# Kernel optimization log

Hardware: AMD Instinct MI355X
Metric: run time of the kernel (lower is better)

Reference implementation:

```python
import jax, jax.numpy as jnp
import numpy as np

VOCAB, EMB = 5000, 300
UNITS = [256, 512, 256]  # two return_sequences layers + final return-last layer
DENSE = 64


def lstm_layer(x, W, U, b, return_seq):
    """Keras-style LSTM with activation='relu', recurrent_activation='sigmoid'.
    x: [B,T,D]; W: [D,4u]; U: [u,4u]; b: [4u]. Gate order: i, f, c, o."""
    B = x.shape[0]
    u = U.shape[0]
    xg = jnp.einsum('btd,dg->btg', x, W) + b  # precompute input projections [B,T,4u]

    def step(carry, xg_t):
        h, c = carry
        g = xg_t + h @ U
        i, f, cc, o = jnp.split(g, 4, axis=-1)
        i = jax.nn.sigmoid(i)
        f = jax.nn.sigmoid(f)
        o = jax.nn.sigmoid(o)
        c = f * c + i * jax.nn.relu(cc)
        h = o * jax.nn.relu(c)
        return (h, c), h

    h0 = jnp.zeros((B, u), x.dtype)
    (hT, _), hs = jax.lax.scan(step, (h0, h0), jnp.swapaxes(xg, 0, 1))
    return jnp.swapaxes(hs, 0, 1) if return_seq else hT


def setup_inputs() -> dict:
    key = jax.random.key(0)
    ks = iter(jax.random.split(key, 16))
    s = 0.05  # small init keeps relu-LSTM numerically stable
    inp = {
        'tokens': jax.random.randint(next(ks), (128, 512), 0, VOCAB, dtype=jnp.int32),
        'emb': jax.random.normal(next(ks), (VOCAB, EMB), jnp.float32) * s,
    }
    d = EMB
    for li, u in enumerate(UNITS):
        inp[f'W{li}'] = jax.random.normal(next(ks), (d, 4 * u), jnp.float32) * s
        inp[f'U{li}'] = jax.random.normal(next(ks), (u, 4 * u), jnp.float32) * s
        inp[f'b{li}'] = jnp.zeros((4 * u,), jnp.float32)
        d = u
    inp['Wd'] = jax.random.normal(next(ks), (UNITS[-1], DENSE), jnp.float32) * s
    inp['bd'] = jnp.zeros((DENSE,), jnp.float32)
    inp['Wc'] = jax.random.normal(next(ks), (DENSE, 1), jnp.float32) * s
    inp['bc'] = jnp.zeros((1,), jnp.float32)
    return inp


def reference(tokens, emb, W0, U0, b0, W1, U1, b1, W2, U2, b2, Wd, bd, Wc, bc):
    x = emb[tokens]                                   # [B,T,300]
    x = lstm_layer(x, W0, U0, b0, return_seq=True)    # [B,T,256]
    x = lstm_layer(x, W1, U1, b1, return_seq=True)    # [B,T,512]
    x = lstm_layer(x, W2, U2, b2, return_seq=False)   # [B,256]
    x = jax.nn.relu(x @ Wd + bd)                      # [B,64]
    return jax.nn.sigmoid(x @ Wc + bc)                # [B,1]
```

## Files before the change

### kernel.cpp

```cpp
#include <hip/hip_runtime.h>
#include <cstdint>
#include <cstddef>

#define BATCH  128
#define SEQT   512
#define EMB_D  300
#define VOCABN 5000
#define KP0    320
#define NU0    256
#define NU1    512
#define NU2    256
#define NDENSE 64
#define RING   32
#define LIM    (1 << 19)

typedef unsigned short ushortT;
typedef unsigned long long ull;
typedef __attribute__((ext_vector_type(8))) short bf16x8;
typedef __attribute__((ext_vector_type(8))) unsigned short u16x8;
typedef __attribute__((ext_vector_type(4))) unsigned short u16x4;
typedef __attribute__((ext_vector_type(4))) float f32x4;

#define AGT __HIP_MEMORY_SCOPE_AGENT

static __device__ __forceinline__ unsigned short f2bf(float x) {
    union { float f; unsigned u; } v; v.f = x;
    const unsigned r = v.u + 0x7FFFu + ((v.u >> 16) & 1u);
    return (unsigned short)(r >> 16);
}
static __device__ __forceinline__ float bf2f(unsigned short b) {
    union { unsigned u; float f; } v; v.u = ((unsigned)b) << 16;
    return v.f;
}
static __device__ __forceinline__ float sigmoidf_(float x) {
    return 1.f / (1.f + __expf(-x));
}
static __device__ __forceinline__ unsigned ald(const unsigned* p) {
    return __hip_atomic_load((unsigned*)p, __ATOMIC_RELAXED, AGT);
}
static __device__ __forceinline__ void ast(unsigned* p, unsigned v) {
    __hip_atomic_store(p, v, __ATOMIC_RELAXED, AGT);
}
static __device__ __forceinline__ void ld16c(u16x8* d, const void* p) {
    asm volatile("global_load_dwordx4 %0, %1, off sc0 sc1"
                 : "=&v"(*d) : "v"(p) : "memory");
}
static __device__ __forceinline__ void ld8c(u16x4* d, const void* p) {
    asm volatile("global_load_dwordx2 %0, %1, off sc0 sc1"
                 : "=&v"(*d) : "v"(p) : "memory");
}
static __device__ __forceinline__ void st4c(void* p, unsigned v) {
    asm volatile("global_store_dword %0, %1, off sc0 sc1"
                 :: "v"(p), "v"(v) : "memory");
}
static __device__ __forceinline__ void wait0() {
    asm volatile("s_waitcnt vmcnt(0)" ::: "memory");
    __builtin_amdgcn_sched_barrier(0);
}
static __device__ __forceinline__ void wait1() {
    asm volatile("s_waitcnt vmcnt(1)" ::: "memory");
    __builtin_amdgcn_sched_barrier(0);
}

__global__ __launch_bounds__(256) void convert_WT(
    const float* __restrict__ W, ushortT* __restrict__ WbfT,
    int K, int NG, int KP, int total)
{
    for (int idx = blockIdx.x * 256 + threadIdx.x; idx < total; idx += gridDim.x * 256) {
        const int m = idx / KP, k = idx - m * KP;
        WbfT[idx] = (k < K) ? f2bf(W[(size_t)k * NG + m]) : (ushortT)0;
    }
}
__global__ __launch_bounds__(256) void convert_emb(
    const float* __restrict__ emb, ushortT* __restrict__ embbf)
{
    const int total = VOCABN * KP0;
    for (int idx = blockIdx.x * 256 + threadIdx.x; idx < total; idx += gridDim.x * 256) {
        const int v = idx / KP0, k = idx - v * KP0;
        embbf[idx] = (k < EMB_D) ? f2bf(emb[(size_t)v * EMB_D + k]) : (ushortT)0;
    }
}

__global__ __launch_bounds__(256) void gemm_xg0(
    const ushortT* __restrict__ embbf,
    const int*   __restrict__ tokens,
    const ushortT* __restrict__ W0T,
    const float* __restrict__ bias,
    ushortT* __restrict__ xg0)
{
    __shared__ ushortT Wl[128][32];
    __shared__ ushortT Xl[128][32];
    __shared__ int tokL[128];

    const int tid = threadIdx.x;
    const int t   = blockIdx.x;
    const int m0  = blockIdx.y * 128;
    const int wv  = tid >> 6;
    const int lane = tid & 63;
    const int lo  = lane & 15;
    const int hi  = lane >> 4;

    if (tid < 128) tokL[tid] = tokens[tid * SEQT + t];
    __syncthreads();

    f32x4 acc[2][8];
    #pragma unroll
    for (int s = 0; s < 2; ++s)
        #pragma unroll
        for (int n = 0; n < 8; ++n)
            acc[s][n] = f32x4{0.f, 0.f, 0.f, 0.f};

    for (int k0 = 0; k0 < KP0; k0 += 32) {
        #pragma unroll
        for (int it = 0; it < 2; ++it) {
            const int idx = tid + it * 256;
            const int row = idx >> 2, gq = idx & 3;
            const int gs  = gq ^ ((row >> 1) & 3);
            *(u16x8*)&Wl[row][gs * 8] =
                *(const u16x8*)(W0T + (size_t)(m0 + row) * KP0 + k0 + gq * 8);
            *(u16x8*)&Xl[row][gs * 8] =
                *(const u16x8*)(embbf + (size_t)tokL[row] * KP0 + k0 + gq * 8);
        }
        __syncthreads();

        bf16x8 bfr[8];
        #pragma unroll
        for (int n = 0; n < 8; ++n) {
            const int row = n * 16 + lo;
            bfr[n] = *(const bf16x8*)&Xl[row][(hi ^ ((row >> 1) & 3)) * 8];
        }
        #pragma unroll
        for (int s = 0; s < 2; ++s) {
            const int row = wv * 32 + s * 16 + lo;
            const bf16x8 a = *(const bf16x8*)&Wl[row][(hi ^ ((row >> 1) & 3)) * 8];
            #pragma unroll
            for (int n = 0; n < 8; ++n)
                acc[s][n] = __builtin_amdgcn_mfma_f32_16x16x32_bf16(a, bfr[n], acc[s][n], 0, 0, 0);
        }
        __syncthreads();
    }

    #pragma unroll
    for (int s = 0; s < 2; ++s)
        #pragma unroll
        for (int j = 0; j < 4; ++j) {
            const int m = m0 + wv * 32 + s * 16 + hi * 4 + j;
            const float bi = bias[m];
            #pragma unroll
            for (int n = 0; n < 8; ++n)
                xg0[(((size_t)t * 8 + n) * 1024 + m) * 16 + lo] = f2bf(acc[s][n][j] + bi);
        }
}

template<int U_, int JCOLS, bool XATOMIC>
__device__ void rec_role(
    int rid,
    const float* __restrict__ Umat,
    const ushortT* __restrict__ xgring, int xmask,
    ushortT* __restrict__ hring,
    unsigned* Fown,
    unsigned* Xown, int xph, int xmsh,
    unsigned* Xguard, int nGd,
    char* smem)
{
    constexpr int NGu   = 4 * U_;
    constexpr int WPG   = U_ / JCOLS;
    constexpr int JH    = JCOLS / 2;
    constexpr int TILES = JH / 16;
    constexpr int KT    = U_ / 32;
    constexpr int GR    = U_ / 8;
    constexpr int NLD   = (16 * GR) / 512;

    ushortT* hstage = (ushortT*)smem;
    float*   ex     = (float*)(smem + 2 * 16 * U_);

    const int tid = threadIdx.x, w = tid >> 6, lane = tid & 63;
    const int lo = lane & 15, hi = lane >> 4;
    const int g4 = w & 3, chh = w >> 2;
    const int grp = rid & 7, wgj = rid >> 3;
    const int b0 = grp * 16, J = wgj * JCOLS;
    const size_t S = (size_t)128 * U_;

    int gc[TILES];
    #pragma unroll
    for (int tl = 0; tl < TILES; ++tl)
        gc[tl] = g4 * U_ + J + chh * JH + tl * 16 + lo;

    bf16x8 bfr[TILES][KT];
    #pragma unroll
    for (int tl = 0; tl < TILES; ++tl)
        #pragma unroll
        for (int kt = 0; kt < KT; ++kt) {
            const float* up = Umat + (size_t)(kt * 32 + hi * 8) * NGu + gc[tl];
            bf16x8 v;
            #pragma unroll
            for (int i = 0; i < 8; ++i) v[i] = (short)f2bf(up[(size_t)i * NGu]);
            bfr[tl][kt] = v;
        }

    float creg[TILES][4];
    #pragma unroll
    for (int tl = 0; tl < TILES; ++tl)
        #pragma unroll
        for (int r = 0; r < 4; ++r) creg[tl][r] = 0.f;

    for (int t = 0; t < SEQT; ++t) {
        if (w == 0) {
            if (t > 0) {
                int guard = 0; bool ok;
                do {
                    bool pred = true;
                    if (lane < 2 * WPG)
                        pred = ((int)ald(&Fown[(grp * 2 * WPG + lane) * 16]) >= t);
                    ok = __all(pred);
                    if (!ok) __builtin_amdgcn_s_sleep(1);
                } while (!ok && ++guard < LIM);
            }
            {
                int guard = 0; bool ok;
                do {
                    bool pred = true;
                    if (XATOMIC && lane < 4) {
                        const int mt = (lane * U_ + J) >> xmsh;
                        const int fi = mt * xph + (t & (xph - 1));
                        pred = ((int)ald(&Xown[fi * 16]) >= t + 1);
                    }
                    for (int i = lane; i < nGd; i += 64)
                        pred = pred && ((int)ald(&Xguard[i * 16]) >= t - (RING - 1));
                    ok = __all(pred);
                    if (!ok) __builtin_amdgcn_s_sleep(8);
                } while (!ok && ++guard < LIM);
            }
        }
        __syncthreads();

        u16x4 xr[TILES];
        const size_t xb = (size_t)((t & xmask) * 8 + grp) * NGu;
        if (XATOMIC) {
            #pragma unroll
            for (int tl = 0; tl < TILES; ++tl)
                ld8c(&xr[tl], xgring + (xb + gc[tl]) * 16 + hi * 4);
        } else {
            #pragma unroll
            for (int tl = 0; tl < TILES; ++tl)
                xr[tl] = *(const u16x4*)(xgring + (xb + gc[tl]) * 16 + hi * 4);
        }
        u16x8 hr[NLD];
        int di[NLD];
        if (t > 0) {
            const ushortT* hsrc = hring + (size_t)((t - 1) & (RING - 1)) * S;
            #pragma unroll
            for (int q = 0; q < NLD; ++q) {
                const int i = tid + q * 512;
                const int row = i / GR, gi = i - row * GR;
                ld16c(&hr[q], hsrc + (size_t)(b0 + row) * U_ + gi * 8);
                di[q] = (row * GR + (gi ^ (row & 7))) * 8;
            }
        }
        if (XATOMIC || t > 0) wait0();
        if (t > 0) {
            #pragma unroll
            for (int q = 0; q < NLD; ++q)
                *(u16x8*)&hstage[di[q]] = hr[q];
        }
        __syncthreads();

        f32x4 acc[TILES];
        #pragma unroll
        for (int tl = 0; tl < TILES; ++tl) acc[tl] = f32x4{0.f, 0.f, 0.f, 0.f};
        if (t > 0) {
            #pragma unroll
            for (int kt = 0; kt < KT; ++kt) {
                const int gs = (kt * 4 + hi) ^ (lo & 7);
                const bf16x8 a = *(const bf16x8*)&hstage[(lo * GR + gs) * 8];
                #pragma unroll
                for (int tl = 0; tl < TILES; ++tl)
                    acc[tl] = __builtin_amdgcn_mfma_f32_16x16x32_bf16(a, bfr[tl][kt], acc[tl], 0, 0, 0);
            }
        }

        float p[TILES][4];
        #pragma unroll
        for (int tl = 0; tl < TILES; ++tl)
            #pragma unroll
            for (int r = 0; r < 4; ++r)
                p[tl][r] = acc[tl][r] + bf2f(xr[tl][r]);

        if (g4 != 2) {
            const int slot = (g4 == 3) ? 2 : g4;
            #pragma unroll
            for (int tl = 0; tl < TILES; ++tl)
                #pragma unroll
                for (int r = 0; r < 4; ++r)
                    ex[((slot * 2 + chh) * JH + tl * 16 + lo) * 17 + hi * 4 + r] = sigmoidf_(p[tl][r]);
        }
        __syncthreads();

        if (g4 == 2) {
            ushortT* hwr = hring + (size_t)(t & (RING - 1)) * S;
            #pragma unroll
            for (int tl = 0; tl < TILES; ++tl) {
                const int jh = tl * 16 + lo;
                const int j  = gc[tl] - 2 * U_;
                unsigned own[4], oth[4];
                #pragma unroll
                for (int r = 0; r < 4; ++r) {
                    const int row = hi * 4 + r;
                    const float i_ = ex[((0 * 2 + chh) * JH + jh) * 17 + row];
                    const float f_ = ex[((1 * 2 + chh) * JH + jh) * 17 + row];
                    const float o_ = ex[((2 * 2 + chh) * JH + jh) * 17 + row];
                    creg[tl][r] = f_ * creg[tl][r] + i_ * fmaxf(p[tl][r], 0.f);
                    const float hn = o_ * fmaxf(creg[tl][r], 0.f);
                    own[r] = (unsigned)f2bf(hn);
                }
                #pragma unroll
                for (int r = 0; r < 4; ++r)
                    oth[r] = (unsigned)__shfl_xor((int)own[r], 1);
                const int odd = lo & 1;
                const int rb = odd ? 2 : 0;
                const int je = j - odd;
                #pragma unroll
                for (int q = 0; q < 2; ++q) {
                    const int r = rb + q;
                    const unsigned pk = odd ? (oth[r] | (own[r] << 16))
                                            : (own[r] | (oth[r] << 16));
                    st4c(&hwr[(size_t)(b0 + hi * 4 + r) * U_ + je], pk);
                }
            }
            wait0();
            if (lane == 0)
                ast(&Fown[((grp * WPG + wgj) * 2 + chh) * 16], (unsigned)(t + 1));
        }
    }
}

template<int MC, int NGATES, int KP, int P>
__device__ void worker_role(
    int mtile, int phase,
    const ushortT* __restrict__ WT,
    const float* __restrict__ bias,
    const ushortT* __restrict__ hring,
    ushortT* __restrict__ xgring,
    unsigned* Fup, int nUp,
    unsigned* Fguard, int nGd,
    unsigned* Xrel,
    char* smem)
{
    constexpr int GR2 = KP / 8;
    constexpr int NIT = KP / 32;
    constexpr int WR  = MC / 8;
    constexpr int MT  = WR / 16;
    ushortT* Wl = (ushortT*)smem;
    ushortT* Xl = (ushortT*)(smem + (size_t)MC * KP * 2);

    const int tid = threadIdx.x, w = tid >> 6, lane = tid & 63;
    const int lo = lane & 15, hi = lane >> 4;
    const int m0 = mtile * MC;
    const int row = tid >> 2, gq = tid & 3;
    const int gsx = gq ^ ((row >> 1) & 3);

    for (int i = tid; i < MC * GR2; i += 512) {
        const int r_ = i / GR2, gi = i - r_ * GR2;
        const int gs = gi ^ (r_ & 7);
        *(u16x8*)&Wl[(r_ * GR2 + gs) * 8] =
            *(const u16x8*)(WT + (size_t)(m0 + r_) * KP + gi * 8);
    }
    float bv[MT][4];
    #pragma unroll
    for (int mt = 0; mt < MT; ++mt)
        #pragma unroll
        for (int j = 0; j < 4; ++j)
            bv[mt][j] = bias[m0 + w * WR + mt * 16 + hi * 4 + j];
    __syncthreads();

    for (int t = phase; t < SEQT; t += P) {
        if (w == 0) {
            int guard = 0; bool ok;
            do {
                bool pred = true;
                for (int i = lane; i < nUp; i += 64)
                    pred = pred && ((int)ald(&Fup[i * 16]) >= t + 1);
                for (int i = lane; i < nGd; i += 64)
                    pred = pred && ((int)ald(&Fguard[i * 16]) >= t - (RING - 1));
                ok = __all(pred);
                if (!ok) __builtin_amdgcn_s_sleep(32);
            } while (!ok && ++guard < LIM);
        }
        __syncthreads();

        const ushortT* hslab = hring + (size_t)(t & (RING - 1)) * 128 * KP;

        f32x4 acc[MT][8];
        #pragma unroll
        for (int mt = 0; mt < MT; ++mt)
            #pragma unroll
            for (int nn = 0; nn < 8; ++nn) acc[mt][nn] = f32x4{0.f, 0.f, 0.f, 0.f};

        u16x8 Ra, Rb;
        ld16c(&Ra, hslab + (size_t)row * KP + gq * 8);
        #pragma unroll
        for (int it = 0; it < NIT; ++it) {
            const bool even = ((it & 1) == 0);
            if (it + 1 < NIT) {
                ld16c(even ? &Rb : &Ra, hslab + (size_t)row * KP + (it + 1) * 32 + gq * 8);
                wait1();
            } else {
                wait0();
            }
            ushortT* Xc = Xl + (it & 1) * (128 * 32);
            *(u16x8*)&Xc[row * 32 + gsx * 8] = even ? Ra : Rb;
            __syncthreads();
            const int k0 = it * 32;
            #pragma unroll
            for (int mt = 0; mt < MT; ++mt) {
                const int arow = w * WR + mt * 16 + lo;
                const int gsa = ((k0 >> 3) + hi) ^ (arow & 7);
                const bf16x8 a = *(const bf16x8*)&Wl[(arow * GR2 + gsa) * 8];
                #pragma unroll
                for (int nn = 0; nn < 8; ++nn) {
                    const int brow = nn * 16 + lo;
                    const bf16x8 b = *(const bf16x8*)&Xc[brow * 32 + (hi ^ ((brow >> 1) & 3)) * 8];
                    acc[mt][nn] = __builtin_amdgcn_mfma_f32_16x16x32_bf16(a, b, acc[mt][nn], 0, 0, 0);
                }
            }
            __syncthreads();
        }

        const size_t slab = (size_t)(t & (RING - 1)) * 8;
        #pragma unroll
        for (int mt = 0; mt < MT; ++mt) {
            #pragma unroll
            for (int nn = 0; nn < 8; ++nn) {
                const int b = nn * 16 + lo;
                unsigned own[4], oth[4];
                #pragma unroll
                for (int j = 0; j < 4; ++j)
                    own[j] = (unsigned)f2bf(acc[mt][nn][j] + bv[mt][j]);
                #pragma unroll
                for (int j = 0; j < 4; ++j)
                    oth[j] = (unsigned)__shfl_xor((int)own[j], 1);
                const int odd = lo & 1;
                const int jb = odd ? 2 : 0;
                const int be = (b & 15) - odd;
                #pragma unroll
                for (int q = 0; q < 2; ++q) {
                    const int j = jb + q;
                    const int m = m0 + w * WR + mt * 16 + hi * 4 + j;
                    const unsigned pk = odd ? (oth[j] | (own[j] << 16))
                                            : (own[j] | (oth[j] << 16));
                    st4c(&xgring[((slab + nn) * NGATES + m) * 16 + be], pk);
                }
            }
        }
        wait0();
        __syncthreads();
        if (tid == 0)
            ast(Xrel, (unsigned)(t + 1));
    }
}

struct MegaArgs {
    const float *U0, *U1, *U2;
    const ushortT *W1T, *W2T;
    const float *b1, *b2;
    const ushortT* xg0;
    ushortT *xg1, *xg2;
    ushortT *h0r, *h1r, *h2r;
    unsigned *F0, *F1, *F2, *X1, *X2;
};

__global__ __launch_bounds__(512, 1) void mega(MegaArgs A)
{
    extern __shared__ char smem[];
    const int bid = blockIdx.x;
    if (bid < 16) {
        rec_role<NU0, 128, false>(bid, A.U0, A.xg0, 511, A.h0r, A.F0,
                                  nullptr, 1, 0, A.X1, 64, smem);
    } else if (bid < 80) {
        rec_role<NU1, 64, true>(bid - 16, A.U1, A.xg1, RING - 1, A.h1r, A.F1,
                                A.X1, 8, 8, A.X2, 32, smem);
    } else if (bid < 96) {
        rec_role<NU2, 128, true>(bid - 80, A.U2, A.xg2, RING - 1, A.h2r, A.F2,
                                 A.X2, 4, 7, nullptr, 0, smem);
    } else if (bid < 160) {
        const int wid = bid - 96;
        const int mt = wid & 7, ph = wid >> 3;
        worker_role<256, 2048, 256, 8>(mt, ph, A.W1T, A.b1, A.h0r, A.xg1,
                                       A.F0, 32, A.F1, 128, A.X1 + (mt * 8 + ph) * 16, smem);
    } else {
        const int wid = bid - 160;
        const int mt = wid & 7, ph = wid >> 3;
        worker_role<128, 1024, 512, 4>(mt, ph, A.W2T, A.b2, A.h1r, A.xg2,
                                       A.F1, 128, A.F2, 32, A.X2 + (mt * 4 + ph) * 16, smem);
    }
}

__global__ __launch_bounds__(64) void head_kernel(
    const ushortT* __restrict__ h2,
    const float* __restrict__ Wd,
    const float* __restrict__ bd,
    const float* __restrict__ Wc,
    const float* __restrict__ bc,
    float* __restrict__ out)
{
    const int b = blockIdx.x;
    const int j = threadIdx.x;
    float a = bd[j];
    const ushortT* hrow = h2 + (size_t)b * NU2;
    #pragma unroll 4
    for (int k = 0; k < NU2; ++k)
        a += bf2f(hrow[k]) * Wd[(size_t)k * NDENSE + j];
    a = fmaxf(a, 0.f) * Wc[j];
    #pragma unroll
    for (int off = 32; off > 0; off >>= 1)
        a += __shfl_down(a, off);
    if (j == 0)
        out[b] = 1.f / (1.f + expf(-(a + bc[0])));
}

extern "C" void kernel_launch(void* const* d_in, const int* in_sizes, int n_in,
                              void* d_out, int out_size, void* d_ws, size_t ws_size,
                              hipStream_t stream)
{
    const int*   tokens = (const int*)  d_in[0];
    const float* emb    = (const float*)d_in[1];
    const float* W0     = (const float*)d_in[2];
    const float* Ur0    = (const float*)d_in[3];
    const float* b0v    = (const float*)d_in[4];
    const float* W1     = (const float*)d_in[5];
    const float* Ur1    = (const float*)d_in[6];
    const float* b1v    = (const float*)d_in[7];
    const float* W2     = (const float*)d_in[8];
    const float* Ur2    = (const float*)d_in[9];
    const float* b2v    = (const float*)d_in[10];
    const float* Wd     = (const float*)d_in[11];
    const float* bd     = (const float*)d_in[12];
    const float* Wc     = (const float*)d_in[13];
    const float* bc     = (const float*)d_in[14];
    float* out = (float*)d_out;

    char* p = (char*)d_ws;
    auto alloc = [&](size_t bytes) -> char* {
        char* q = p; p += (bytes + 255) & ~(size_t)255; return q;
    };
    ushortT* xg0   = (ushortT*)alloc((size_t)SEQT * 8 * 1024 * 16 * 2);
    ushortT* xg1   = (ushortT*)alloc((size_t)RING * 8 * 2048 * 16 * 2);
    ushortT* xg2   = (ushortT*)alloc((size_t)RING * 8 * 1024 * 16 * 2);
    ushortT* h0r   = (ushortT*)alloc((size_t)RING * 128 * NU0 * 2);
    ushortT* h1r   = (ushortT*)alloc((size_t)RING * 128 * NU1 * 2);
    ushortT* h2r   = (ushortT*)alloc((size_t)RING * 128 * NU2 * 2);
    ushortT* W0T   = (ushortT*)alloc((size_t)1024 * KP0 * 2);
    ushortT* W1T   = (ushortT*)alloc((size_t)2048 * NU0 * 2);
    ushortT* W2T   = (ushortT*)alloc((size_t)1024 * NU1 * 2);
    ushortT* embbf = (ushortT*)alloc((size_t)VOCABN * KP0 * 2);
    unsigned* flg  = (unsigned*)alloc(32768);

    unsigned* F0 = flg;
    unsigned* F1 = F0 + 32 * 16;
    unsigned* F2 = F1 + 128 * 16;
    unsigned* X1 = F2 + 32 * 16;
    unsigned* X2 = X1 + 64 * 16;

    hipMemsetAsync(flg, 0, 32768, stream);

    convert_WT<<<512, 256, 0, stream>>>(W0, W0T, EMB_D, 1024, KP0, 1024 * KP0);
    convert_WT<<<512, 256, 0, stream>>>(W1, W1T, NU0, 2048, NU0, 2048 * NU0);
    convert_WT<<<512, 256, 0, stream>>>(W2, W2T, NU1, 1024, NU1, 1024 * NU1);
    convert_emb<<<1024, 256, 0, stream>>>(emb, embbf);

    gemm_xg0<<<dim3(SEQT, 8), 256, 0, stream>>>(embbf, tokens, W0T, b0v, xg0);

    MegaArgs A;
    A.U0 = Ur0; A.U1 = Ur1; A.U2 = Ur2;
    A.W1T = W1T; A.W2T = W2T;
    A.b1 = b1v; A.b2 = b2v;
    A.xg0 = xg0; A.xg1 = xg1; A.xg2 = xg2;
    A.h0r = h0r; A.h1r = h1r; A.h2r = h2r;
    A.F0 = F0; A.F1 = F1; A.F2 = F2; A.X1 = X1; A.X2 = X2;

    void* args[] = {&A};
    hipLaunchCooperativeKernel((void*)mega, dim3(192), dim3(512), args, 147456, stream);

    head_kernel<<<BATCH, 64, 0, stream>>>(h2r + (size_t)31 * 128 * NU2,
                                          Wd, bd, Wc, bc, out);
}
```

Baseline: 2.813 ms.

## Restructure recurrent blocks so each wave owns all four gates per column

Each recurrent workgroup shrinks to 256 threads and 64 hidden columns, and each wave now computes all four gate tiles for its 16 columns. The cell update happens in registers, with no LDS exchange of sigmoid values and no extra barrier. The input-projection slice for step t+1 is prefetched during step t and the X-flag poll is merged into the single per-step wait loop. The grid grows from 192 to 224 blocks, and the workers are adjusted to 256 threads with two loads per thread and flag counts halved. This trades more blocks and more cross-block flag polling for a shorter per-step critical path within each block.

```diff
diff --git a/kernel.cpp b/kernel.cpp
--- a/kernel.cpp
+++ b/kernel.cpp
@@ -57,8 +57,8 @@
     asm volatile("s_waitcnt vmcnt(0)" ::: "memory");
     __builtin_amdgcn_sched_barrier(0);
 }
-static __device__ __forceinline__ void wait1() {
-    asm volatile("s_waitcnt vmcnt(1)" ::: "memory");
+static __device__ __forceinline__ void wait2() {
+    asm volatile("s_waitcnt vmcnt(2)" ::: "memory");
     __builtin_amdgcn_sched_barrier(0);
 }
 
@@ -152,185 +152,169 @@
         }
 }
 
-template<int U_, int JCOLS, bool XATOMIC>
+template<int U_, bool XATOMIC, int XTSH, int XPH>
 __device__ void rec_role(
     int rid,
     const float* __restrict__ Umat,
     const ushortT* __restrict__ xgring, int xmask,
     ushortT* __restrict__ hring,
     unsigned* Fown,
-    unsigned* Xown, int xph, int xmsh,
+    unsigned* Xown,
     unsigned* Xguard, int nGd,
     char* smem)
 {
-    constexpr int NGu   = 4 * U_;
-    constexpr int WPG   = U_ / JCOLS;
-    constexpr int JH    = JCOLS / 2;
-    constexpr int TILES = JH / 16;
-    constexpr int KT    = U_ / 32;
-    constexpr int GR    = U_ / 8;
-    constexpr int NLD   = (16 * GR) / 512;
+    constexpr int NGu = 4 * U_;
+    constexpr int WPG = U_ / 64;
+    constexpr int KT  = U_ / 32;
+    constexpr int GR  = U_ / 8;
+    constexpr int NLD = (16 * GR) / 256;
 
     ushortT* hstage = (ushortT*)smem;
-    float*   ex     = (float*)(smem + 2 * 16 * U_);
 
     const int tid = threadIdx.x, w = tid >> 6, lane = tid & 63;
     const int lo = lane & 15, hi = lane >> 4;
-    const int g4 = w & 3, chh = w >> 2;
     const int grp = rid & 7, wgj = rid >> 3;
-    const int b0 = grp * 16, J = wgj * JCOLS;
+    const int b0 = grp * 16, J = wgj * 64;
+    const int jcol = J + w * 16 + lo;
     const size_t S = (size_t)128 * U_;
 
-    int gc[TILES];
+    bf16x8 bfr[4][KT];
     #pragma unroll
-    for (int tl = 0; tl < TILES; ++tl)
-        gc[tl] = g4 * U_ + J + chh * JH + tl * 16 + lo;
-
-    bf16x8 bfr[TILES][KT];
-    #pragma unroll
-    for (int tl = 0; tl < TILES; ++tl)
+    for (int g = 0; g < 4; ++g)
         #pragma unroll
         for (int kt = 0; kt < KT; ++kt) {
-            const float* up = Umat + (size_t)(kt * 32 + hi * 8) * NGu + gc[tl];
+            const float* up = Umat + (size_t)(kt * 32 + hi * 8) * NGu + g * U_ + jcol;
             bf16x8 v;
             #pragma unroll
             for (int i = 0; i < 8; ++i) v[i] = (short)f2bf(up[(size_t)i * NGu]);
-            bfr[tl][kt] = v;
-        }
-
-    float creg[TILES][4];
-    #pragma unroll
-    for (int tl = 0; tl < TILES; ++tl)
-        #pragma unroll
-        for (int r = 0; r < 4; ++r) creg[tl][r] = 0.f;
+            bfr[g][kt] = v;
+        }
+
+    float creg[4] = {0.f, 0.f, 0.f, 0.f};
+
+    if (XATOMIC) {
+        if (w == 0) {
+            int guard = 0; bool ok;
+            do {
+                bool pred = true;
+                if (lane < 4) {
+                    const int mt = (lane * U_ + J) >> XTSH;
+                    pred = ((int)ald(&Xown[(mt * XPH) * 16]) >= 1);
+                }
+                ok = __all(pred);
+                if (!ok) __builtin_amdgcn_s_sleep(2);
+            } while (!ok && ++guard < LIM);
+        }
+        __syncthreads();
+    }
+    u16x4 xnext[4];
+    {
+        const size_t xb = (size_t)grp * NGu;
+        #pragma unroll
+        for (int g = 0; g < 4; ++g) {
+            const ushortT* ap = xgring + (xb + g * U_ + jcol) * 16 + hi * 4;
+            if (XATOMIC) ld8c(&xnext[g], ap);
+            else         xnext[g] = *(const u16x4*)ap;
+        }
+        if (XATOMIC) wait0();
+    }
 
     for (int t = 0; t < SEQT; ++t) {
         if (w == 0) {
-            if (t > 0) {
-                int guard = 0; bool ok;
-                do {
-                    bool pred = true;
-                    if (lane < 2 * WPG)
-                        pred = ((int)ald(&Fown[(grp * 2 * WPG + lane) * 16]) >= t);
-                    ok = __all(pred);
-                    if (!ok) __builtin_amdgcn_s_sleep(1);
-                } while (!ok && ++guard < LIM);
-            }
-            {
-                int guard = 0; bool ok;
-                do {
-                    bool pred = true;
-                    if (XATOMIC && lane < 4) {
-                        const int mt = (lane * U_ + J) >> xmsh;
-                        const int fi = mt * xph + (t & (xph - 1));
-                        pred = ((int)ald(&Xown[fi * 16]) >= t + 1);
-                    }
-                    for (int i = lane; i < nGd; i += 64)
-                        pred = pred && ((int)ald(&Xguard[i * 16]) >= t - (RING - 1));
-                    ok = __all(pred);
-                    if (!ok) __builtin_amdgcn_s_sleep(8);
-                } while (!ok && ++guard < LIM);
-            }
-        }
-        __syncthreads();
-
-        u16x4 xr[TILES];
-        const size_t xb = (size_t)((t & xmask) * 8 + grp) * NGu;
-        if (XATOMIC) {
-            #pragma unroll
-            for (int tl = 0; tl < TILES; ++tl)
-                ld8c(&xr[tl], xgring + (xb + gc[tl]) * 16 + hi * 4);
-        } else {
-            #pragma unroll
-            for (int tl = 0; tl < TILES; ++tl)
-                xr[tl] = *(const u16x4*)(xgring + (xb + gc[tl]) * 16 + hi * 4);
-        }
+            int guard = 0; bool ok;
+            do {
+                bool pred = true;
+                if (t > 0 && lane < WPG)
+                    pred = ((int)ald(&Fown[(grp * WPG + lane) * 16]) >= t);
+                if (XATOMIC && t + 1 < SEQT && lane < 4) {
+                    const int mt = (lane * U_ + J) >> XTSH;
+                    const int fi = mt * XPH + ((t + 1) & (XPH - 1));
+                    pred = pred && ((int)ald(&Xown[fi * 16]) >= t + 2);
+                }
+                for (int i = lane; i < nGd; i += 64)
+                    pred = pred && ((int)ald(&Xguard[i * 16]) >= t - (RING - 1));
+                ok = __all(pred);
+                if (!ok) __builtin_amdgcn_s_sleep(1);
+            } while (!ok && ++guard < LIM);
+        }
+        __syncthreads();
+
+        u16x4 xcur[4];
+        #pragma unroll
+        for (int g = 0; g < 4; ++g) xcur[g] = xnext[g];
+
         u16x8 hr[NLD];
-        int di[NLD];
         if (t > 0) {
             const ushortT* hsrc = hring + (size_t)((t - 1) & (RING - 1)) * S;
             #pragma unroll
             for (int q = 0; q < NLD; ++q) {
-                const int i = tid + q * 512;
+                const int i = tid + q * 256;
                 const int row = i / GR, gi = i - row * GR;
                 ld16c(&hr[q], hsrc + (size_t)(b0 + row) * U_ + gi * 8);
-                di[q] = (row * GR + (gi ^ (row & 7))) * 8;
-            }
-        }
-        if (XATOMIC || t > 0) wait0();
-        if (t > 0) {
-            #pragma unroll
-            for (int q = 0; q < NLD; ++q)
-                *(u16x8*)&hstage[di[q]] = hr[q];
-        }
-        __syncthreads();
-
-        f32x4 acc[TILES];
-        #pragma unroll
-        for (int tl = 0; tl < TILES; ++tl) acc[tl] = f32x4{0.f, 0.f, 0.f, 0.f};
+            }
+            wait0();
+            #pragma unroll
+            for (int q = 0; q < NLD; ++q) {
+                const int i = tid + q * 256;
+                const int row = i / GR, gi = i - row * GR;
+                *(u16x8*)&hstage[(row * GR + (gi ^ (row & 7))) * 8] = hr[q];
+            }
+        }
+        if (t + 1 < SEQT) {
+            const size_t xb = (size_t)(((t + 1) & xmask) * 8 + grp) * NGu;
+            #pragma unroll
+            for (int g = 0; g < 4; ++g) {
+                const ushortT* ap = xgring + (xb + g * U_ + jcol) * 16 + hi * 4;
+                if (XATOMIC) ld8c(&xnext[g], ap);
+                else         xnext[g] = *(const u16x4*)ap;
+            }
+        }
+        __syncthreads();
+
+        f32x4 acc[4];
+        #pragma unroll
+        for (int g = 0; g < 4; ++g) acc[g] = f32x4{0.f, 0.f, 0.f, 0.f};
         if (t > 0) {
             #pragma unroll
             for (int kt = 0; kt < KT; ++kt) {
                 const int gs = (kt * 4 + hi) ^ (lo & 7);
                 const bf16x8 a = *(const bf16x8*)&hstage[(lo * GR + gs) * 8];
                 #pragma unroll
-                for (int tl = 0; tl < TILES; ++tl)
-                    acc[tl] = __builtin_amdgcn_mfma_f32_16x16x32_bf16(a, bfr[tl][kt], acc[tl], 0, 0, 0);
-            }
-        }
-
-        float p[TILES][4];
-        #pragma unroll
-        for (int tl = 0; tl < TILES; ++tl)
-            #pragma unroll
-            for (int r = 0; r < 4; ++r)
-                p[tl][r] = acc[tl][r] + bf2f(xr[tl][r]);
-
-        if (g4 != 2) {
-            const int slot = (g4 == 3) ? 2 : g4;
-            #pragma unroll
-            for (int tl = 0; tl < TILES; ++tl)
-                #pragma unroll
-                for (int r = 0; r < 4; ++r)
-                    ex[((slot * 2 + chh) * JH + tl * 16 + lo) * 17 + hi * 4 + r] = sigmoidf_(p[tl][r]);
-        }
-        __syncthreads();
-
-        if (g4 == 2) {
-            ushortT* hwr = hring + (size_t)(t & (RING - 1)) * S;
-            #pragma unroll
-            for (int tl = 0; tl < TILES; ++tl) {
-                const int jh = tl * 16 + lo;
-                const int j  = gc[tl] - 2 * U_;
-                unsigned own[4], oth[4];
-                #pragma unroll
-                for (int r = 0; r < 4; ++r) {
-                    const int row = hi * 4 + r;
-                    const float i_ = ex[((0 * 2 + chh) * JH + jh) * 17 + row];
-                    const float f_ = ex[((1 * 2 + chh) * JH + jh) * 17 + row];
-                    const float o_ = ex[((2 * 2 + chh) * JH + jh) * 17 + row];
-                    creg[tl][r] = f_ * creg[tl][r] + i_ * fmaxf(p[tl][r], 0.f);
-                    const float hn = o_ * fmaxf(creg[tl][r], 0.f);
-                    own[r] = (unsigned)f2bf(hn);
-                }
-                #pragma unroll
-                for (int r = 0; r < 4; ++r)
-                    oth[r] = (unsigned)__shfl_xor((int)own[r], 1);
-                const int odd = lo & 1;
-                const int rb = odd ? 2 : 0;
-                const int je = j - odd;
-                #pragma unroll
-                for (int q = 0; q < 2; ++q) {
-                    const int r = rb + q;
-                    const unsigned pk = odd ? (oth[r] | (own[r] << 16))
-                                            : (own[r] | (oth[r] << 16));
-                    st4c(&hwr[(size_t)(b0 + hi * 4 + r) * U_ + je], pk);
-                }
-            }
-            wait0();
-            if (lane == 0)
-                ast(&Fown[((grp * WPG + wgj) * 2 + chh) * 16], (unsigned)(t + 1));
-        }
+                for (int g = 0; g < 4; ++g)
+                    acc[g] = __builtin_amdgcn_mfma_f32_16x16x32_bf16(a, bfr[g][kt], acc[g], 0, 0, 0);
+            }
+        }
+
+        ushortT* hwr = hring + (size_t)(t & (RING - 1)) * S;
+        unsigned own[4], oth[4];
+        #pragma unroll
+        for (int r = 0; r < 4; ++r) {
+            const float i_ = sigmoidf_(acc[0][r] + bf2f(xcur[0][r]));
+            const float f_ = sigmoidf_(acc[1][r] + bf2f(xcur[1][r]));
+            const float cc = fmaxf(acc[2][r] + bf2f(xcur[2][r]), 0.f);
+            const float o_ = sigmoidf_(acc[3][r] + bf2f(xcur[3][r]));
+            creg[r] = f_ * creg[r] + i_ * cc;
+            own[r] = (unsigned)f2bf(o_ * fmaxf(creg[r], 0.f));
+        }
+        #pragma unroll
+        for (int r = 0; r < 4; ++r)
+            oth[r] = (unsigned)__shfl_xor((int)own[r], 1);
+        {
+            const int odd = lo & 1;
+            const int rb = odd ? 2 : 0;
+            const int je = jcol - odd;
+            #pragma unroll
+            for (int q = 0; q < 2; ++q) {
+                const int r = rb + q;
+                const unsigned pk = odd ? (oth[r] | (own[r] << 16))
+                                        : (own[r] | (oth[r] << 16));
+                st4c(&hwr[(size_t)(b0 + hi * 4 + r) * U_ + je], pk);
+            }
+        }
+        wait0();
+        __syncthreads();
+        if (tid == 0)
+            ast(&Fown[(grp * WPG + wgj) * 16], (unsigned)(t + 1));
     }
 }
 
@@ -348,7 +332,7 @@
 {
     constexpr int GR2 = KP / 8;
     constexpr int NIT = KP / 32;
-    constexpr int WR  = MC / 8;
+    constexpr int WR  = MC / 4;
     constexpr int MT  = WR / 16;
     ushortT* Wl = (ushortT*)smem;
     ushortT* Xl = (ushortT*)(smem + (size_t)MC * KP * 2);
@@ -356,10 +340,11 @@
     const int tid = threadIdx.x, w = tid >> 6, lane = tid & 63;
     const int lo = lane & 15, hi = lane >> 4;
     const int m0 = mtile * MC;
-    const int row = tid >> 2, gq = tid & 3;
-    const int gsx = gq ^ ((row >> 1) & 3);
-
-    for (int i = tid; i < MC * GR2; i += 512) {
+    const int row = tid >> 1, gq0 = (tid & 1) * 2;
+    const int gs0 = gq0 ^ ((row >> 1) & 3);
+    const int gs1 = (gq0 + 1) ^ ((row >> 1) & 3);
+
+    for (int i = tid; i < MC * GR2; i += 256) {
         const int r_ = i / GR2, gi = i - r_ * GR2;
         const int gs = gi ^ (r_ & 7);
         *(u16x8*)&Wl[(r_ * GR2 + gs) * 8] =
@@ -396,25 +381,28 @@
             #pragma unroll
             for (int nn = 0; nn < 8; ++nn) acc[mt][nn] = f32x4{0.f, 0.f, 0.f, 0.f};
 
-        u16x8 Ra, Rb;
-        ld16c(&Ra, hslab + (size_t)row * KP + gq * 8);
+        u16x8 Ra0, Ra1, Rb0, Rb1;
+        ld16c(&Ra0, hslab + (size_t)row * KP + gq0 * 8);
+        ld16c(&Ra1, hslab + (size_t)row * KP + (gq0 + 1) * 8);
         #pragma unroll
         for (int it = 0; it < NIT; ++it) {
             const bool even = ((it & 1) == 0);
             if (it + 1 < NIT) {
-                ld16c(even ? &Rb : &Ra, hslab + (size_t)row * KP + (it + 1) * 32 + gq * 8);
-                wait1();
+                const ushortT* np = hslab + (size_t)row * KP + (it + 1) * 32;
+                if (even) { ld16c(&Rb0, np + gq0 * 8); ld16c(&Rb1, np + (gq0 + 1) * 8); }
+                else      { ld16c(&Ra0, np + gq0 * 8); ld16c(&Ra1, np + (gq0 + 1) * 8); }
+                wait2();
             } else {
                 wait0();
             }
             ushortT* Xc = Xl + (it & 1) * (128 * 32);
-            *(u16x8*)&Xc[row * 32 + gsx * 8] = even ? Ra : Rb;
+            *(u16x8*)&Xc[row * 32 + gs0 * 8] = even ? Ra0 : Rb0;
+            *(u16x8*)&Xc[row * 32 + gs1 * 8] = even ? Ra1 : Rb1;
             __syncthreads();
-            const int k0 = it * 32;
             #pragma unroll
             for (int mt = 0; mt < MT; ++mt) {
                 const int arow = w * WR + mt * 16 + lo;
-                const int gsa = ((k0 >> 3) + hi) ^ (arow & 7);
+                const int gsa = (it * 4 + hi) ^ (arow & 7);
                 const bf16x8 a = *(const bf16x8*)&Wl[(arow * GR2 + gsa) * 8];
                 #pragma unroll
                 for (int nn = 0; nn < 8; ++nn) {
@@ -469,29 +457,29 @@
     unsigned *F0, *F1, *F2, *X1, *X2;
 };
 
-__global__ __launch_bounds__(512, 1) void mega(MegaArgs A)
+__global__ __launch_bounds__(256, 1) void mega(MegaArgs A)
 {
     extern __shared__ char smem[];
     const int bid = blockIdx.x;
-    if (bid < 16) {
-        rec_role<NU0, 128, false>(bid, A.U0, A.xg0, 511, A.h0r, A.F0,
-                                  nullptr, 1, 0, A.X1, 64, smem);
-    } else if (bid < 80) {
-        rec_role<NU1, 64, true>(bid - 16, A.U1, A.xg1, RING - 1, A.h1r, A.F1,
-                                A.X1, 8, 8, A.X2, 32, smem);
+    if (bid < 32) {
+        rec_role<NU0, false, 1, 1>(bid, A.U0, A.xg0, 511, A.h0r, A.F0,
+                                   nullptr, A.X1, 64, smem);
     } else if (bid < 96) {
-        rec_role<NU2, 128, true>(bid - 80, A.U2, A.xg2, RING - 1, A.h2r, A.F2,
-                                 A.X2, 4, 7, nullptr, 0, smem);
-    } else if (bid < 160) {
-        const int wid = bid - 96;
+        rec_role<NU1, true, 8, 8>(bid - 32, A.U1, A.xg1, RING - 1, A.h1r, A.F1,
+                                  A.X1, A.X2, 32, smem);
+    } else if (bid < 128) {
+        rec_role<NU2, true, 7, 4>(bid - 96, A.U2, A.xg2, RING - 1, A.h2r, A.F2,
+                                  A.X2, nullptr, 0, smem);
+    } else if (bid < 192) {
+        const int wid = bid - 128;
         const int mt = wid & 7, ph = wid >> 3;
         worker_role<256, 2048, 256, 8>(mt, ph, A.W1T, A.b1, A.h0r, A.xg1,
-                                       A.F0, 32, A.F1, 128, A.X1 + (mt * 8 + ph) * 16, smem);
+                                       A.F0, 32, A.F1, 64, A.X1 + (mt * 8 + ph) * 16, smem);
     } else {
-        const int wid = bid - 160;
+        const int wid = bid - 192;
         const int mt = wid & 7, ph = wid >> 3;
         worker_role<128, 1024, 512, 4>(mt, ph, A.W2T, A.b2, A.h1r, A.xg2,
-                                       A.F1, 128, A.F2, 32, A.X2 + (mt * 4 + ph) * 16, smem);
+                                       A.F1, 64, A.F2, 32, A.X2 + (mt * 4 + ph) * 16, smem);
     }
 }
 
@@ -557,7 +545,7 @@
 
     unsigned* F0 = flg;
     unsigned* F1 = F0 + 32 * 16;
-    unsigned* F2 = F1 + 128 * 16;
+    unsigned* F2 = F1 + 64 * 16;
     unsigned* X1 = F2 + 32 * 16;
     unsigned* X2 = X1 + 64 * 16;
 
@@ -579,7 +567,7 @@
     A.F0 = F0; A.F1 = F1; A.F2 = F2; A.X1 = X1; A.X2 = X2;
 
     void* args[] = {&A};
-    hipLaunchCooperativeKernel((void*)mega, dim3(192), dim3(512), args, 147456, stream);
+    hipLaunchCooperativeKernel((void*)mega, dim3(224), dim3(256), args, 147456, stream);
 
     head_kernel<<<BATCH, 64, 0, stream>>>(h2r + (size_t)31 * 128 * NU2,
                                           Wd, bd, Wc, bc, out);
```

After: 2.461 ms. 12.5% less time.
